# Optimization experiments

Measured on AMD Instinct MI355X. Metric: run time of the kernel, lower is better.

The kernel has to match this reference:

```python
import jax, jax.numpy as jnp
import numpy as np

N_NODES = 50000
N_EDGES = 600000
IN_C = 128
HID = 128
OUT_C = 32
N_GRAPHS = 64


def setup_inputs() -> dict:
    key = jax.random.key(0)
    ks = jax.random.split(key, 12)
    x = jax.random.normal(ks[0], (N_NODES, IN_C), dtype=jnp.float32)
    edge_index = jax.random.randint(ks[1], (2, N_EDGES), 0, N_NODES, dtype=jnp.int64)
    batch = jnp.sort(jax.random.randint(ks[2], (N_NODES,), 0, N_GRAPHS, dtype=jnp.int64))
    s1 = 1.0 / np.sqrt(IN_C)
    s2 = 1.0 / np.sqrt(HID)
    # SAGEConv: out = lin_l(mean_neighbors) + lin_r(x); lin_l has bias, lin_r has none
    W1l = jax.random.uniform(ks[3], (HID, IN_C), minval=-s1, maxval=s1, dtype=jnp.float32)
    b1 = jax.random.uniform(ks[4], (HID,), minval=-s1, maxval=s1, dtype=jnp.float32)
    W1r = jax.random.uniform(ks[5], (HID, IN_C), minval=-s1, maxval=s1, dtype=jnp.float32)
    W2l = jax.random.uniform(ks[6], (HID, HID), minval=-s2, maxval=s2, dtype=jnp.float32)
    b2 = jax.random.uniform(ks[7], (HID,), minval=-s2, maxval=s2, dtype=jnp.float32)
    W2r = jax.random.uniform(ks[8], (HID, HID), minval=-s2, maxval=s2, dtype=jnp.float32)
    Wlin = jax.random.uniform(ks[9], (OUT_C, HID), minval=-s2, maxval=s2, dtype=jnp.float32)
    blin = jax.random.uniform(ks[10], (OUT_C,), minval=-s2, maxval=s2, dtype=jnp.float32)
    return {"x": x, "edge_index": edge_index, "batch": batch,
            "W1l": W1l, "b1": b1, "W1r": W1r,
            "W2l": W2l, "b2": b2, "W2r": W2r,
            "Wlin": Wlin, "blin": blin}


def _sage_conv(x, src, dst, Wl, bl, Wr):
    # mean aggregation of source-node features onto destination nodes
    msg_sum = jax.ops.segment_sum(x[src], dst, num_segments=N_NODES)  # [N, d]
    deg = jax.ops.segment_sum(jnp.ones((src.shape[0],), x.dtype), dst, num_segments=N_NODES)
    mean = msg_sum / jnp.maximum(deg, 1.0)[:, None]
    return mean @ Wl.T + bl + x @ Wr.T


def reference(x, edge_index, batch, W1l, b1, W1r, W2l, b2, W2r, Wlin, blin):
    src, dst = edge_index[0], edge_index[1]
    h = jax.nn.relu(_sage_conv(x, src, dst, W1l, b1, W1r))
    h = jax.nn.relu(_sage_conv(h, src, dst, W2l, b2, W2r))
    # global mean pool over graph ids
    gsum = jax.ops.segment_sum(h, batch, num_segments=N_GRAPHS)        # [G, HID]
    cnt = jax.ops.segment_sum(jnp.ones((h.shape[0],), h.dtype), batch, num_segments=N_GRAPHS)
    pooled = gsum / jnp.maximum(cnt, 1.0)[:, None]
    return pooled @ Wlin.T + blin
```

## Files before the change

### kernel.cpp

```cpp
#include <hip/hip_runtime.h>
#include <hip/hip_fp16.h>

#define N_NODES 50000
#define N_EDGES 600000
#define N_GRAPHS 64
#define HID 128
#define OUT_C 32

#define SCAN_BLK 256
#define N_SCAN_BLOCKS ((N_NODES + SCAN_BLK - 1) / SCAN_BLK)

typedef __attribute__((ext_vector_type(8))) short short8;
typedef __attribute__((ext_vector_type(8))) unsigned short ushort8;
typedef __attribute__((ext_vector_type(4))) float f32x4;

__global__ void build_w_bf16(const float* __restrict__ Wl, const float* __restrict__ Wr,
                             unsigned short* __restrict__ Whn, unsigned short* __restrict__ Wln) {
    int idx = blockIdx.x * 256 + threadIdx.x;
    int n = idx >> 8, k = idx & 255;
    float a = (k < 128) ? Wl[n * 128 + k] : Wr[n * 128 + (k - 128)];
    unsigned int u = __float_as_uint(a);
    float hf = __uint_as_float(u & 0xFFFF0000u);
    float lf = a - hf;
    Whn[idx] = (unsigned short)(u >> 16);
    Wln[idx] = (unsigned short)(__float_as_uint(lf) >> 16);
}

__global__ void cast_f16(const float* __restrict__ in, __half* __restrict__ out, int n) {
    int i = (blockIdx.x * 256 + threadIdx.x) * 4;
    if (i < n) {
        float4 v = *(const float4*)(in + i);
        __half2 a = __floats2half2_rn(v.x, v.y);
        __half2 b = __floats2half2_rn(v.z, v.w);
        uint2 st;
        st.x = *(const unsigned int*)&a;
        st.y = *(const unsigned int*)&b;
        *(uint2*)(out + i) = st;
    }
}

__global__ void deg_kernel(const int* __restrict__ dst, int* __restrict__ deg, int E) {
    int e = blockIdx.x * 256 + threadIdx.x;
    if (e < E) atomicAdd(&deg[dst[e]], 1);
}

__global__ __launch_bounds__(SCAN_BLK) void scan_blocksum(
    const int* __restrict__ deg, int* __restrict__ bsum) {
    __shared__ int s[SCAN_BLK];
    int i = blockIdx.x * SCAN_BLK + threadIdx.x;
    s[threadIdx.x] = (i < N_NODES) ? deg[i] : 0;
    __syncthreads();
    for (int off = SCAN_BLK / 2; off > 0; off >>= 1) {
        if (threadIdx.x < off) s[threadIdx.x] += s[threadIdx.x + off];
        __syncthreads();
    }
    if (threadIdx.x == 0) bsum[blockIdx.x] = s[0];
}

__global__ __launch_bounds__(256) void scan_boff(
    const int* __restrict__ bsum, int* __restrict__ boff, int* __restrict__ rowptr) {
    __shared__ int s[256];
    int t = threadIdx.x;
    int v = (t < N_SCAN_BLOCKS) ? bsum[t] : 0;
    s[t] = v;
    __syncthreads();
    for (int off = 1; off < 256; off <<= 1) {
        int u = (t >= off) ? s[t - off] : 0;
        __syncthreads();
        s[t] += u;
        __syncthreads();
    }
    if (t < N_SCAN_BLOCKS) boff[t] = s[t] - v;
    if (t == N_SCAN_BLOCKS - 1) rowptr[N_NODES] = s[t];
}

__global__ __launch_bounds__(SCAN_BLK) void scan_emit(
    const int* __restrict__ deg, const int* __restrict__ boff,
    int* __restrict__ rowptr, float* __restrict__ invdeg) {
    __shared__ int s[SCAN_BLK];
    int i = blockIdx.x * SCAN_BLK + threadIdx.x;
    int t = threadIdx.x;
    int v = (i < N_NODES) ? deg[i] : 0;
    s[t] = v;
    __syncthreads();
    for (int off = 1; off < SCAN_BLK; off <<= 1) {
        int u = (t >= off) ? s[t - off] : 0;
        __syncthreads();
        s[t] += u;
        __syncthreads();
    }
    if (i < N_NODES) {
        rowptr[i] = boff[blockIdx.x] + s[t] - v;
        invdeg[i] = 1.0f / fmaxf((float)v, 1.0f);
    }
}

__global__ void fill_kernel(const int* __restrict__ src, const int* __restrict__ dst,
                            const int* __restrict__ rowptr, int* __restrict__ cursor,
                            int* __restrict__ eidx, int E) {
    int e = blockIdx.x * 256 + threadIdx.x;
    if (e < E) {
        int d = dst[e];
        int pos = atomicAdd(&cursor[d], 1);
        eidx[rowptr[d] + pos] = src[e];
    }
}

__global__ __launch_bounds__(256) void aggregate_f16(
    const __half* __restrict__ feat16, const int* __restrict__ rowptr,
    const int* __restrict__ eidx, const float* __restrict__ invdeg,
    float* __restrict__ mean) {
    const int node = blockIdx.x * 4 + (threadIdx.x >> 6);
    if (node >= N_NODES) return;
    const int lane = threadIdx.x & 63;
    const int beg = rowptr[node];
    const int end = rowptr[node + 1];
    const size_t coff = (size_t)lane * 2;

    float2 a0 = {0.f, 0.f}, a1 = {0.f, 0.f}, a2 = {0.f, 0.f}, a3 = {0.f, 0.f};
    int i = beg;
    for (; i + 8 <= end; i += 8) {
        int s0 = eidx[i + 0], s1 = eidx[i + 1], s2 = eidx[i + 2], s3 = eidx[i + 3];
        int s4 = eidx[i + 4], s5 = eidx[i + 5], s6 = eidx[i + 6], s7 = eidx[i + 7];
        __half2 v0 = *(const __half2*)(feat16 + (size_t)s0 * 128 + coff);
        __half2 v1 = *(const __half2*)(feat16 + (size_t)s1 * 128 + coff);
        __half2 v2 = *(const __half2*)(feat16 + (size_t)s2 * 128 + coff);
        __half2 v3 = *(const __half2*)(feat16 + (size_t)s3 * 128 + coff);
        __half2 v4 = *(const __half2*)(feat16 + (size_t)s4 * 128 + coff);
        __half2 v5 = *(const __half2*)(feat16 + (size_t)s5 * 128 + coff);
        __half2 v6 = *(const __half2*)(feat16 + (size_t)s6 * 128 + coff);
        __half2 v7 = *(const __half2*)(feat16 + (size_t)s7 * 128 + coff);
        float2 f0 = __half22float2(v0), f1 = __half22float2(v1);
        float2 f2 = __half22float2(v2), f3 = __half22float2(v3);
        float2 f4 = __half22float2(v4), f5 = __half22float2(v5);
        float2 f6 = __half22float2(v6), f7 = __half22float2(v7);
        a0.x += f0.x; a0.y += f0.y;  a1.x += f1.x; a1.y += f1.y;
        a2.x += f2.x; a2.y += f2.y;  a3.x += f3.x; a3.y += f3.y;
        a0.x += f4.x; a0.y += f4.y;  a1.x += f5.x; a1.y += f5.y;
        a2.x += f6.x; a2.y += f6.y;  a3.x += f7.x; a3.y += f7.y;
    }
    if (i + 4 <= end) {
        int s0 = eidx[i + 0], s1 = eidx[i + 1], s2 = eidx[i + 2], s3 = eidx[i + 3];
        __half2 v0 = *(const __half2*)(feat16 + (size_t)s0 * 128 + coff);
        __half2 v1 = *(const __half2*)(feat16 + (size_t)s1 * 128 + coff);
        __half2 v2 = *(const __half2*)(feat16 + (size_t)s2 * 128 + coff);
        __half2 v3 = *(const __half2*)(feat16 + (size_t)s3 * 128 + coff);
        float2 f0 = __half22float2(v0), f1 = __half22float2(v1);
        float2 f2 = __half22float2(v2), f3 = __half22float2(v3);
        a0.x += f0.x; a0.y += f0.y;  a1.x += f1.x; a1.y += f1.y;
        a2.x += f2.x; a2.y += f2.y;  a3.x += f3.x; a3.y += f3.y;
        i += 4;
    }
    if (i + 2 <= end) {
        int s0 = eidx[i + 0], s1 = eidx[i + 1];
        __half2 v0 = *(const __half2*)(feat16 + (size_t)s0 * 128 + coff);
        __half2 v1 = *(const __half2*)(feat16 + (size_t)s1 * 128 + coff);
        float2 f0 = __half22float2(v0), f1 = __half22float2(v1);
        a0.x += f0.x; a0.y += f0.y;  a1.x += f1.x; a1.y += f1.y;
        i += 2;
    }
    if (i < end) {
        int s0 = eidx[i];
        float2 f0 = __half22float2(*(const __half2*)(feat16 + (size_t)s0 * 128 + coff));
        a0.x += f0.x; a0.y += f0.y;
    }

    const float sc = invdeg[node];
    float2 acc;
    acc.x = ((a0.x + a1.x) + (a2.x + a3.x)) * sc;
    acc.y = ((a0.y + a1.y) + (a2.y + a3.y)) * sc;
    *(float2*)(mean + (size_t)node * 128 + lane * 2) = acc;
}

#define GBM 64
#define GBK 32
#define ASTR 48
#define BSTR 48

__global__ __launch_bounds__(256) void sage_gemm_mfma(
    const float* __restrict__ mean, const float* __restrict__ feat,
    const unsigned short* __restrict__ Whn, const unsigned short* __restrict__ Wln,
    const float* __restrict__ bias, float* __restrict__ out,
    __half* __restrict__ out16, int M) {
    __shared__ __align__(16) unsigned short Ah[GBM][ASTR];
    __shared__ __align__(16) unsigned short Al[GBM][ASTR];
    __shared__ __align__(16) unsigned short Bh[128][BSTR];
    __shared__ __align__(16) unsigned short Bl[128][BSTR];

    const int tid = threadIdx.x;
    const int wave = tid >> 6;
    const int lane = tid & 63;
    const int l15 = lane & 15;
    const int quad = lane >> 4;
    const int row0 = blockIdx.x * GBM;

    f32x4 acc[8];
#pragma unroll
    for (int t = 0; t < 8; ++t) acc[t] = (f32x4){0.f, 0.f, 0.f, 0.f};

    const int ar = tid >> 2;
    const int ac = (tid & 3) * 8;

    for (int k0 = 0; k0 < 256; k0 += GBK) {
        {
            int gi = row0 + ar;
            float va[8];
            if (gi < M) {
                const float* p = (k0 < 128) ? (mean + (size_t)gi * 128 + k0 + ac)
                                            : (feat + (size_t)gi * 128 + (k0 - 128) + ac);
                float4 v0 = *(const float4*)p;
                float4 v1 = *(const float4*)(p + 4);
                va[0] = v0.x; va[1] = v0.y; va[2] = v0.z; va[3] = v0.w;
                va[4] = v1.x; va[5] = v1.y; va[6] = v1.z; va[7] = v1.w;
            } else {
#pragma unroll
                for (int i = 0; i < 8; ++i) va[i] = 0.f;
            }
            ushort8 h, l;
#pragma unroll
            for (int i = 0; i < 8; ++i) {
                unsigned int u = __float_as_uint(va[i]);
                float hf = __uint_as_float(u & 0xFFFF0000u);
                float lf = va[i] - hf;
                h[i] = (unsigned short)(u >> 16);
                l[i] = (unsigned short)(__float_as_uint(lf) >> 16);
            }
            *(ushort8*)&Ah[ar][ac] = h;
            *(ushort8*)&Al[ar][ac] = l;
        }
#pragma unroll
        for (int i = 0; i < 2; ++i) {
            int id = tid + i * 256;
            int n = id >> 2;
            int kc = (id & 3) * 8;
            *(ushort8*)&Bh[n][kc] = *(const ushort8*)(Whn + (size_t)n * 256 + k0 + kc);
            *(ushort8*)&Bl[n][kc] = *(const ushort8*)(Wln + (size_t)n * 256 + k0 + kc);
        }
        __syncthreads();

        const short8 a_h = *(const short8*)&Ah[wave * 16 + l15][quad * 8];
        const short8 a_l = *(const short8*)&Al[wave * 16 + l15][quad * 8];
#pragma unroll
        for (int t = 0; t < 8; ++t) {
            const short8 b_h = *(const short8*)&Bh[t * 16 + l15][quad * 8];
            const short8 b_l = *(const short8*)&Bl[t * 16 + l15][quad * 8];
            acc[t] = __builtin_amdgcn_mfma_f32_16x16x32_bf16(a_h, b_h, acc[t], 0, 0, 0);
            acc[t] = __builtin_amdgcn_mfma_f32_16x16x32_bf16(a_h, b_l, acc[t], 0, 0, 0);
            acc[t] = __builtin_amdgcn_mfma_f32_16x16x32_bf16(a_l, b_h, acc[t], 0, 0, 0);
        }
        __syncthreads();
    }

#pragma unroll
    for (int r = 0; r < 4; ++r) {
        int gi = row0 + wave * 16 + quad * 4 + r;
        if (gi < M) {
#pragma unroll
            for (int t = 0; t < 8; ++t) {
                int col = t * 16 + l15;
                float v = fmaxf(acc[t][r] + bias[col], 0.f);
                out[(size_t)gi * 128 + col] = v;
                if (out16) out16[(size_t)gi * 128 + col] = __float2half(v);
            }
        }
    }
}

#define POOL_PARTS 4
__global__ __launch_bounds__(256) void pool_graph(
    const float* __restrict__ h, const int* __restrict__ batch,
    float* __restrict__ pooled, int* __restrict__ gcnt) {
    const int g = blockIdx.x >> 2;
    const int part = blockIdx.x & 3;
    int lo = 0, hi = N_NODES;
    while (lo < hi) { int mid = (lo + hi) >> 1; if (batch[mid] < g) lo = mid + 1; else hi = mid; }
    const int start = lo;
    hi = N_NODES;
    while (lo < hi) { int mid = (lo + hi) >> 1; if (batch[mid] < g + 1) lo = mid + 1; else hi = mid; }
    const int end = lo;

    const int t = threadIdx.x;
    if (part == 0 && t == 0) gcnt[g] = end - start;

    const int c4 = (t & 31) * 4;
    const int rg = t >> 5;
    float4 acc = {0.f, 0.f, 0.f, 0.f};
    for (int n = start + part * 8 + rg; n < end; n += 8 * POOL_PARTS) {
        float4 v = *(const float4*)(h + (size_t)n * 128 + c4);
        acc.x += v.x; acc.y += v.y; acc.z += v.z; acc.w += v.w;
    }
    __shared__ float sm[8][132];
    sm[rg][c4 + 0] = acc.x;
    sm[rg][c4 + 1] = acc.y;
    sm[rg][c4 + 2] = acc.z;
    sm[rg][c4 + 3] = acc.w;
    __syncthreads();
    if (t < 128) {
        float s = 0.f;
#pragma unroll
        for (int r = 0; r < 8; ++r) s += sm[r][t];
        atomicAdd(&pooled[g * 128 + t], s);
    }
}

__global__ void final_kernel(const float* __restrict__ pooled, const int* __restrict__ gcnt,
                             const float* __restrict__ Wlin, const float* __restrict__ blin,
                             float* __restrict__ out) {
    int g = blockIdx.x;
    int j = threadIdx.x;
    float inv = 1.0f / fmaxf((float)gcnt[g], 1.0f);
    float sum = blin[j];
    const float* prow = pooled + g * 128;
    const float* wrow = Wlin + j * 128;
    for (int c = 0; c < 128; ++c) sum += prow[c] * inv * wrow[c];
    out[g * 32 + j] = sum;
}

extern "C" void kernel_launch(void* const* d_in, const int* in_sizes, int n_in,
                              void* d_out, int out_size, void* d_ws, size_t ws_size,
                              hipStream_t stream) {
    const float* x    = (const float*)d_in[0];
    const int*   src  = (const int*)d_in[1];
    const int*   dst  = ((const int*)d_in[1]) + N_EDGES;
    const int*   batch= (const int*)d_in[2];
    const float* W1l  = (const float*)d_in[3];
    const float* b1   = (const float*)d_in[4];
    const float* W1r  = (const float*)d_in[5];
    const float* W2l  = (const float*)d_in[6];
    const float* b2   = (const float*)d_in[7];
    const float* W2r  = (const float*)d_in[8];
    const float* Wlin = (const float*)d_in[9];
    const float* blin = (const float*)d_in[10];
    float* out = (float*)d_out;

    float* ws      = (float*)d_ws;
    float* mean    = ws;
    float* h1      = mean + 6400000;
    float* h2      = h1 + 6400000;
    __half* xh     = (__half*)(h2 + 6400000);
    float* pooled  = (float*)(xh + 6400000);
    int*   gcnt    = (int*)(pooled + N_GRAPHS * 128);
    float* invdeg  = (float*)(gcnt + 64);
    unsigned short* Whn1 = (unsigned short*)(invdeg + N_NODES);
    unsigned short* Wln1 = Whn1 + 32768;
    unsigned short* Whn2 = Wln1 + 32768;
    unsigned short* Wln2 = Whn2 + 32768;
    int*   degi    = (int*)(Wln2 + 32768);
    int*   cursor  = degi + N_NODES;
    int*   rowptr  = cursor + N_NODES;
    int*   eidx    = rowptr + N_NODES + 1;
    int*   bsum    = eidx + N_EDGES;
    int*   boff    = bsum + N_SCAN_BLOCKS;

    hipMemsetAsync(degi, 0, (size_t)(2 * N_NODES) * sizeof(int), stream);
    hipMemsetAsync(pooled, 0, (size_t)(N_GRAPHS * 128) * sizeof(float), stream);

    build_w_bf16<<<128, 256, 0, stream>>>(W1l, W1r, Whn1, Wln1);
    build_w_bf16<<<128, 256, 0, stream>>>(W2l, W2r, Whn2, Wln2);
    cast_f16<<<(N_NODES * 128 / 4 + 255) / 256, 256, 0, stream>>>(x, xh, N_NODES * 128);

    deg_kernel<<<(N_EDGES + 255) / 256, 256, 0, stream>>>(dst, degi, N_EDGES);
    scan_blocksum<<<N_SCAN_BLOCKS, SCAN_BLK, 0, stream>>>(degi, bsum);
    scan_boff<<<1, 256, 0, stream>>>(bsum, boff, rowptr);
    scan_emit<<<N_SCAN_BLOCKS, SCAN_BLK, 0, stream>>>(degi, boff, rowptr, invdeg);
    fill_kernel<<<(N_EDGES + 255) / 256, 256, 0, stream>>>(src, dst, rowptr, cursor, eidx, N_EDGES);

    const int gemm_grid = (N_NODES + GBM - 1) / GBM;

    aggregate_f16<<<(N_NODES + 3) / 4, 256, 0, stream>>>(xh, rowptr, eidx, invdeg, mean);
    sage_gemm_mfma<<<gemm_grid, 256, 0, stream>>>(mean, x, Whn1, Wln1, b1, h1, xh, N_NODES);

    aggregate_f16<<<(N_NODES + 3) / 4, 256, 0, stream>>>(xh, rowptr, eidx, invdeg, mean);
    sage_gemm_mfma<<<gemm_grid, 256, 0, stream>>>(mean, h1, Whn2, Wln2, b2, h2,
                                                  (__half*)nullptr, N_NODES);

    pool_graph<<<N_GRAPHS * POOL_PARTS, 256, 0, stream>>>(h2, batch, pooled, gcnt);
    final_kernel<<<N_GRAPHS, 32, 0, stream>>>(pooled, gcnt, Wlin, blin, out);
}
```

Measured before the change: 283.4 us.

## Store all intermediate activations in fp16 and feed GEMM A operand directly

```diff
diff --git a/kernel.cpp b/kernel.cpp
--- a/kernel.cpp
+++ b/kernel.cpp
@@ -10,20 +10,18 @@
 #define SCAN_BLK 256
 #define N_SCAN_BLOCKS ((N_NODES + SCAN_BLK - 1) / SCAN_BLK)
 
-typedef __attribute__((ext_vector_type(8))) short short8;
-typedef __attribute__((ext_vector_type(8))) unsigned short ushort8;
+typedef __attribute__((ext_vector_type(8))) _Float16 half8;
 typedef __attribute__((ext_vector_type(4))) float f32x4;
 
-__global__ void build_w_bf16(const float* __restrict__ Wl, const float* __restrict__ Wr,
-                             unsigned short* __restrict__ Whn, unsigned short* __restrict__ Wln) {
+__global__ void build_w_f16(const float* __restrict__ Wlw, const float* __restrict__ Wrw,
+                            __half* __restrict__ Wh, __half* __restrict__ Wl) {
     int idx = blockIdx.x * 256 + threadIdx.x;
     int n = idx >> 8, k = idx & 255;
-    float a = (k < 128) ? Wl[n * 128 + k] : Wr[n * 128 + (k - 128)];
-    unsigned int u = __float_as_uint(a);
-    float hf = __uint_as_float(u & 0xFFFF0000u);
-    float lf = a - hf;
-    Whn[idx] = (unsigned short)(u >> 16);
-    Wln[idx] = (unsigned short)(__float_as_uint(lf) >> 16);
+    float a = (k < 128) ? Wlw[n * 128 + k] : Wrw[n * 128 + (k - 128)];
+    __half hh = __float2half(a);
+    float hf = __half2float(hh);
+    Wh[idx] = hh;
+    Wl[idx] = __float2half(a - hf);
 }
 
 __global__ void cast_f16(const float* __restrict__ in, __half* __restrict__ out, int n) {
@@ -109,7 +107,7 @@
 __global__ __launch_bounds__(256) void aggregate_f16(
     const __half* __restrict__ feat16, const int* __restrict__ rowptr,
     const int* __restrict__ eidx, const float* __restrict__ invdeg,
-    float* __restrict__ mean) {
+    __half* __restrict__ mean16) {
     const int node = blockIdx.x * 4 + (threadIdx.x >> 6);
     if (node >= N_NODES) return;
     const int lane = threadIdx.x & 63;
@@ -166,26 +164,20 @@
     }
 
     const float sc = invdeg[node];
-    float2 acc;
-    acc.x = ((a0.x + a1.x) + (a2.x + a3.x)) * sc;
-    acc.y = ((a0.y + a1.y) + (a2.y + a3.y)) * sc;
-    *(float2*)(mean + (size_t)node * 128 + lane * 2) = acc;
+    float mx = ((a0.x + a1.x) + (a2.x + a3.x)) * sc;
+    float my = ((a0.y + a1.y) + (a2.y + a3.y)) * sc;
+    *(__half2*)(mean16 + (size_t)node * 128 + lane * 2) = __floats2half2_rn(mx, my);
 }
 
 #define GBM 64
-#define GBK 32
-#define ASTR 48
 #define BSTR 48
 
-__global__ __launch_bounds__(256) void sage_gemm_mfma(
-    const float* __restrict__ mean, const float* __restrict__ feat,
-    const unsigned short* __restrict__ Whn, const unsigned short* __restrict__ Wln,
-    const float* __restrict__ bias, float* __restrict__ out,
-    __half* __restrict__ out16, int M) {
-    __shared__ __align__(16) unsigned short Ah[GBM][ASTR];
-    __shared__ __align__(16) unsigned short Al[GBM][ASTR];
-    __shared__ __align__(16) unsigned short Bh[128][BSTR];
-    __shared__ __align__(16) unsigned short Bl[128][BSTR];
+__global__ __launch_bounds__(256) void sage_gemm_f16(
+    const __half* __restrict__ mean16, const __half* __restrict__ feat16,
+    const __half* __restrict__ Wh, const __half* __restrict__ Wl,
+    const float* __restrict__ bias, __half* __restrict__ out16, int M) {
+    __shared__ __align__(16) __half Bh[128][BSTR];
+    __shared__ __align__(16) __half Bl[128][BSTR];
 
     const int tid = threadIdx.x;
     const int wave = tid >> 6;
@@ -193,60 +185,41 @@
     const int l15 = lane & 15;
     const int quad = lane >> 4;
     const int row0 = blockIdx.x * GBM;
+    const int gi_a = min(row0 + wave * 16 + l15, M - 1);
+
+    half8 af[8];
+#pragma unroll
+    for (int kb = 0; kb < 8; ++kb) {
+        const int k0 = kb * 32;
+        const __half* ap = (k0 < 128)
+            ? (mean16 + (size_t)gi_a * 128 + k0 + quad * 8)
+            : (feat16 + (size_t)gi_a * 128 + (k0 - 128) + quad * 8);
+        af[kb] = *(const half8*)ap;
+    }
 
     f32x4 acc[8];
 #pragma unroll
     for (int t = 0; t < 8; ++t) acc[t] = (f32x4){0.f, 0.f, 0.f, 0.f};
 
-    const int ar = tid >> 2;
-    const int ac = (tid & 3) * 8;
-
-    for (int k0 = 0; k0 < 256; k0 += GBK) {
-        {
-            int gi = row0 + ar;
-            float va[8];
-            if (gi < M) {
-                const float* p = (k0 < 128) ? (mean + (size_t)gi * 128 + k0 + ac)
-                                            : (feat + (size_t)gi * 128 + (k0 - 128) + ac);
-                float4 v0 = *(const float4*)p;
-                float4 v1 = *(const float4*)(p + 4);
-                va[0] = v0.x; va[1] = v0.y; va[2] = v0.z; va[3] = v0.w;
-                va[4] = v1.x; va[5] = v1.y; va[6] = v1.z; va[7] = v1.w;
-            } else {
-#pragma unroll
-                for (int i = 0; i < 8; ++i) va[i] = 0.f;
-            }
-            ushort8 h, l;
-#pragma unroll
-            for (int i = 0; i < 8; ++i) {
-                unsigned int u = __float_as_uint(va[i]);
-                float hf = __uint_as_float(u & 0xFFFF0000u);
-                float lf = va[i] - hf;
-                h[i] = (unsigned short)(u >> 16);
-                l[i] = (unsigned short)(__float_as_uint(lf) >> 16);
-            }
-            *(ushort8*)&Ah[ar][ac] = h;
-            *(ushort8*)&Al[ar][ac] = l;
-        }
+#pragma unroll
+    for (int kb = 0; kb < 8; ++kb) {
+        const int k0 = kb * 32;
 #pragma unroll
         for (int i = 0; i < 2; ++i) {
             int id = tid + i * 256;
             int n = id >> 2;
             int kc = (id & 3) * 8;
-            *(ushort8*)&Bh[n][kc] = *(const ushort8*)(Whn + (size_t)n * 256 + k0 + kc);
-            *(ushort8*)&Bl[n][kc] = *(const ushort8*)(Wln + (size_t)n * 256 + k0 + kc);
+            *(half8*)&Bh[n][kc] = *(const half8*)(Wh + (size_t)n * 256 + k0 + kc);
+            *(half8*)&Bl[n][kc] = *(const half8*)(Wl + (size_t)n * 256 + k0 + kc);
         }
         __syncthreads();
 
-        const short8 a_h = *(const short8*)&Ah[wave * 16 + l15][quad * 8];
-        const short8 a_l = *(const short8*)&Al[wave * 16 + l15][quad * 8];
 #pragma unroll
         for (int t = 0; t < 8; ++t) {
-            const short8 b_h = *(const short8*)&Bh[t * 16 + l15][quad * 8];
-            const short8 b_l = *(const short8*)&Bl[t * 16 + l15][quad * 8];
-            acc[t] = __builtin_amdgcn_mfma_f32_16x16x32_bf16(a_h, b_h, acc[t], 0, 0, 0);
-            acc[t] = __builtin_amdgcn_mfma_f32_16x16x32_bf16(a_h, b_l, acc[t], 0, 0, 0);
-            acc[t] = __builtin_amdgcn_mfma_f32_16x16x32_bf16(a_l, b_h, acc[t], 0, 0, 0);
+            const half8 b_h = *(const half8*)&Bh[t * 16 + l15][quad * 8];
+            const half8 b_l = *(const half8*)&Bl[t * 16 + l15][quad * 8];
+            acc[t] = __builtin_amdgcn_mfma_f32_16x16x32_f16(af[kb], b_h, acc[t], 0, 0, 0);
+            acc[t] = __builtin_amdgcn_mfma_f32_16x16x32_f16(af[kb], b_l, acc[t], 0, 0, 0);
         }
         __syncthreads();
     }
@@ -259,8 +232,7 @@
             for (int t = 0; t < 8; ++t) {
                 int col = t * 16 + l15;
                 float v = fmaxf(acc[t][r] + bias[col], 0.f);
-                out[(size_t)gi * 128 + col] = v;
-                if (out16) out16[(size_t)gi * 128 + col] = __float2half(v);
+                out16[(size_t)gi * 128 + col] = __float2half(v);
             }
         }
     }
@@ -268,7 +240,7 @@
 
 #define POOL_PARTS 4
 __global__ __launch_bounds__(256) void pool_graph(
-    const float* __restrict__ h, const int* __restrict__ batch,
+    const __half* __restrict__ h, const int* __restrict__ batch,
     float* __restrict__ pooled, int* __restrict__ gcnt) {
     const int g = blockIdx.x >> 2;
     const int part = blockIdx.x & 3;
@@ -286,8 +258,10 @@
     const int rg = t >> 5;
     float4 acc = {0.f, 0.f, 0.f, 0.f};
     for (int n = start + part * 8 + rg; n < end; n += 8 * POOL_PARTS) {
-        float4 v = *(const float4*)(h + (size_t)n * 128 + c4);
-        acc.x += v.x; acc.y += v.y; acc.z += v.z; acc.w += v.w;
+        const __half2* p = (const __half2*)(h + (size_t)n * 128 + c4);
+        float2 f0 = __half22float2(p[0]);
+        float2 f1 = __half22float2(p[1]);
+        acc.x += f0.x; acc.y += f0.y; acc.z += f1.x; acc.w += f1.y;
     }
     __shared__ float sm[8][132];
     sm[rg][c4 + 0] = acc.x;
@@ -333,19 +307,18 @@
     const float* blin = (const float*)d_in[10];
     float* out = (float*)d_out;
 
-    float* ws      = (float*)d_ws;
-    float* mean    = ws;
-    float* h1      = mean + 6400000;
-    float* h2      = h1 + 6400000;
-    __half* xh     = (__half*)(h2 + 6400000);
-    float* pooled  = (float*)(xh + 6400000);
+    __half* xh     = (__half*)d_ws;
+    __half* mean16 = xh + 6400000;
+    __half* h1_16  = mean16 + 6400000;
+    __half* h2_16  = h1_16 + 6400000;
+    __half* Wh1    = h2_16 + 6400000;
+    __half* Wl1    = Wh1 + 32768;
+    __half* Wh2    = Wl1 + 32768;
+    __half* Wl2    = Wh2 + 32768;
+    float* pooled  = (float*)(Wl2 + 32768);
     int*   gcnt    = (int*)(pooled + N_GRAPHS * 128);
     float* invdeg  = (float*)(gcnt + 64);
-    unsigned short* Whn1 = (unsigned short*)(invdeg + N_NODES);
-    unsigned short* Wln1 = Whn1 + 32768;
-    unsigned short* Whn2 = Wln1 + 32768;
-    unsigned short* Wln2 = Whn2 + 32768;
-    int*   degi    = (int*)(Wln2 + 32768);
+    int*   degi    = (int*)(invdeg + N_NODES);
     int*   cursor  = degi + N_NODES;
     int*   rowptr  = cursor + N_NODES;
     int*   eidx    = rowptr + N_NODES + 1;
@@ -355,8 +328,8 @@
     hipMemsetAsync(degi, 0, (size_t)(2 * N_NODES) * sizeof(int), stream);
     hipMemsetAsync(pooled, 0, (size_t)(N_GRAPHS * 128) * sizeof(float), stream);
 
-    build_w_bf16<<<128, 256, 0, stream>>>(W1l, W1r, Whn1, Wln1);
-    build_w_bf16<<<128, 256, 0, stream>>>(W2l, W2r, Whn2, Wln2);
+    build_w_f16<<<128, 256, 0, stream>>>(W1l, W1r, Wh1, Wl1);
+    build_w_f16<<<128, 256, 0, stream>>>(W2l, W2r, Wh2, Wl2);
     cast_f16<<<(N_NODES * 128 / 4 + 255) / 256, 256, 0, stream>>>(x, xh, N_NODES * 128);
 
     deg_kernel<<<(N_EDGES + 255) / 256, 256, 0, stream>>>(dst, degi, N_EDGES);
@@ -367,13 +340,12 @@
 
     const int gemm_grid = (N_NODES + GBM - 1) / GBM;
 
-    aggregate_f16<<<(N_NODES + 3) / 4, 256, 0, stream>>>(xh, rowptr, eidx, invdeg, mean);
-    sage_gemm_mfma<<<gemm_grid, 256, 0, stream>>>(mean, x, Whn1, Wln1, b1, h1, xh, N_NODES);
-
-    aggregate_f16<<<(N_NODES + 3) / 4, 256, 0, stream>>>(xh, rowptr, eidx, invdeg, mean);
-    sage_gemm_mfma<<<gemm_grid, 256, 0, stream>>>(mean, h1, Whn2, Wln2, b2, h2,
-                                                  (__half*)nullptr, N_NODES);
-
-    pool_graph<<<N_GRAPHS * POOL_PARTS, 256, 0, stream>>>(h2, batch, pooled, gcnt);
+    aggregate_f16<<<(N_NODES + 3) / 4, 256, 0, stream>>>(xh, rowptr, eidx, invdeg, mean16);
+    sage_gemm_f16<<<gemm_grid, 256, 0, stream>>>(mean16, xh, Wh1, Wl1, b1, h1_16, N_NODES);
+
+    aggregate_f16<<<(N_NODES + 3) / 4, 256, 0, stream>>>(h1_16, rowptr, eidx, invdeg, mean16);
+    sage_gemm_f16<<<gemm_grid, 256, 0, stream>>>(mean16, h1_16, Wh2, Wl2, b2, h2_16, N_NODES);
+
+    pool_graph<<<N_GRAPHS * POOL_PARTS, 256, 0, stream>>>(h2_16, batch, pooled, gcnt);
     final_kernel<<<N_GRAPHS, 32, 0, stream>>>(pooled, gcnt, Wlin, blin, out);
 }
```

After: 272.3 us. -3.9%, faster.
